# Optimization experiments

Measured on AMD Instinct MI355X. Metric: run time of the kernel, lower is better.

The kernel has to match this reference:

```python
import jax, jax.numpy as jnp
import numpy as np

NUM_GRAPHS = 512


def gcn_conv(x, W, b, src, dst, deg_inv_sqrt, n_nodes):
    # PyG GCNConv: out = D^{-1/2} (A+I) D^{-1/2} X W + b
    h = x @ W                                             # [N, F_out]
    norm = deg_inv_sqrt[src] * deg_inv_sqrt[dst]          # [E]
    msg = h[src] * norm[:, None]                          # gather + scale, [E, F_out]
    agg = jax.ops.segment_sum(msg, dst, num_segments=n_nodes)
    agg = agg + h * (deg_inv_sqrt ** 2)[:, None]          # self-loop term (norm = 1/deg)
    return agg + b


def setup_inputs() -> dict:
    key = jax.random.key(0)
    ks = jax.random.split(key, 8)
    N, E, F_in = 50000, 800000, 256
    hid2, out = 128, 64
    x = jax.random.normal(ks[0], (N, F_in), dtype=jnp.float32)
    edge_index = jax.random.randint(ks[1], (2, E), 0, N, dtype=jnp.int32)
    batch = jnp.sort(jax.random.randint(ks[2], (N,), 0, NUM_GRAPHS, dtype=jnp.int32))
    s = lambda k, sh: jax.random.normal(k, sh, dtype=jnp.float32) * (1.0 / np.sqrt(sh[0]))
    return {
        "x": x,
        "edge_index": edge_index,
        "batch": batch,
        "W1": s(ks[3], (F_in, hid2)), "b1": jnp.zeros((hid2,), jnp.float32),
        "W3": s(ks[4], (hid2, out)), "b3": jnp.zeros((out,), jnp.float32),
        "W4": s(ks[5], (hid2, out)), "b4": jnp.zeros((out,), jnp.float32),
        "Wfc": s(ks[6], (out, 4)), "bfc": jnp.zeros((4,), jnp.float32),
        "noise": jax.random.normal(ks[7], (N, out), dtype=jnp.float32),
    }


def reference(x, edge_index, batch, W1, b1, W3, b3, W4, b4, Wfc, bfc, noise):
    n_nodes = x.shape[0]
    src, dst = edge_index[0], edge_index[1]
    # degree of A + I (count of incoming edges per dst, plus self-loop)
    deg = jax.ops.segment_sum(jnp.ones_like(src, dtype=x.dtype), dst,
                              num_segments=n_nodes) + 1.0
    deg_inv_sqrt = jax.lax.rsqrt(deg)

    h = jax.nn.relu(gcn_conv(x, W1, b1, src, dst, deg_inv_sqrt, n_nodes))  # dropout p=0
    mean = gcn_conv(h, W3, b3, src, dst, deg_inv_sqrt, n_nodes)
    log_std = gcn_conv(h, W4, b4, src, dst, deg_inv_sqrt, n_nodes)
    z = mean + noise * jnp.exp(log_std)                   # reparametrize (training=True)

    # scatter_mean over graph ids
    sums = jax.ops.segment_sum(z, batch, num_segments=NUM_GRAPHS)
    counts = jax.ops.segment_sum(jnp.ones((n_nodes,), z.dtype), batch,
                                 num_segments=NUM_GRAPHS)
    pooled = sums / jnp.maximum(counts, 1.0)[:, None]     # [G, out]

    logits = pooled @ Wfc + bfc                           # [G, 4]
    return jax.nn.log_softmax(logits, axis=1)
```

## Files before the change

kernel.cpp:

```cpp
#include <hip/hip_runtime.h>
#include <hip/hip_bf16.h>
#include <cstdint>
#include <cmath>


typedef __attribute__((ext_vector_type(8))) short bf16x8;
typedef __attribute__((ext_vector_type(4))) float f32x4;

__device__ __forceinline__ unsigned short f2bf(float f) {
    union { float f; unsigned u; } v; v.f = f;
    unsigned u = v.u;
    return (unsigned short)((u + 0x7fffu + ((u >> 16) & 1u)) >> 16);
}
__device__ __forceinline__ float bf2f(unsigned b) {
    union { float f; unsigned u; } v; v.u = b << 16; return v.f;
}
__device__ __forceinline__ unsigned packbf(float lo, float hi) {
    return (unsigned)f2bf(lo) | ((unsigned)f2bf(hi) << 16);
}

__global__ __launch_bounds__(256) void deg_kernel(const int* __restrict__ dst,
                                                  int* __restrict__ deg, int E) {
    int e = blockIdx.x * 256 + threadIdx.x;
    if (e < E) atomicAdd(&deg[dst[e]], 1);
}

__global__ __launch_bounds__(256) void scan1_kernel(const int* __restrict__ deg,
                                                    int* __restrict__ bsum, int N) {
    int t = threadIdx.x;
    int base = blockIdx.x * 1024 + t * 4;
    int s = 0;
    if (base + 3 < N) {
        int4 v = *(const int4*)(deg + base);
        s = v.x + v.y + v.z + v.w;
    } else {
        for (int i = 0; i < 4; i++) if (base + i < N) s += deg[base + i];
    }
    __shared__ int red[256];
    red[t] = s;
    __syncthreads();
    for (int off = 128; off > 0; off >>= 1) {
        if (t < off) red[t] += red[t + off];
        __syncthreads();
    }
    if (t == 0) bsum[blockIdx.x] = red[0];
}

__global__ __launch_bounds__(256) void scan2_kernel(int* __restrict__ bsum, int nb) {
    __shared__ int s[256];
    int t = threadIdx.x;
    s[t] = (t < nb) ? bsum[t] : 0;
    __syncthreads();
    for (int off = 1; off < 256; off <<= 1) {
        int u = (t >= off) ? s[t - off] : 0;
        __syncthreads();
        s[t] += u;
        __syncthreads();
    }
    if (t < nb) bsum[t] = (t == 0) ? 0 : s[t - 1];
}

__global__ __launch_bounds__(256) void scan3_kernel(const int* __restrict__ deg,
                                                    const int* __restrict__ bsum,
                                                    int* __restrict__ offs,
                                                    int* __restrict__ cursor,
                                                    float* __restrict__ dis,
                                                    int N, int E) {
    int t = threadIdx.x;
    int bid = blockIdx.x;
    int base = bid * 1024 + t * 4;
    int d[4] = {0, 0, 0, 0};
    if (base + 3 < N) {
        int4 v = *(const int4*)(deg + base);
        d[0] = v.x; d[1] = v.y; d[2] = v.z; d[3] = v.w;
    } else {
        for (int i = 0; i < 4; i++) if (base + i < N) d[i] = deg[base + i];
    }
    int s = d[0] + d[1] + d[2] + d[3];
    __shared__ int red[256];
    red[t] = s;
    __syncthreads();
    for (int off = 1; off < 256; off <<= 1) {
        int u = (t >= off) ? red[t - off] : 0;
        __syncthreads();
        red[t] += u;
        __syncthreads();
    }
    int run = bsum[bid] + ((t == 0) ? 0 : red[t - 1]);
#pragma unroll
    for (int i = 0; i < 4; i++) {
        int idx = base + i;
        if (idx < N) {
            offs[idx] = run;
            cursor[idx] = run;
            dis[idx] = rsqrtf((float)d[i] + 1.0f);
            run += d[i];
        }
    }
    if (bid == 0 && t == 0) offs[N] = E;
}

__global__ __launch_bounds__(256) void fill_kernel(const int* __restrict__ src,
                                                   const int* __restrict__ dst,
                                                   int* __restrict__ cursor,
                                                   int* __restrict__ adj, int E) {
    int e = blockIdx.x * 256 + threadIdx.x;
    if (e >= E) return;
    int pos = atomicAdd(&cursor[dst[e]], 1);
    adj[pos] = src[e];
}

__global__ __launch_bounds__(256) void wt_kernel(const float* __restrict__ W,
                                                 unsigned short* __restrict__ wT) {
    int idx = blockIdx.x * 256 + threadIdx.x;
    if (idx < 32768) {
        int k = idx >> 7;
        int c = idx & 127;
        wT[c * 256 + k] = f2bf(W[idx]);
    }
}

__global__ __launch_bounds__(256) void gemm1_mfma(const float* __restrict__ x,
                                                  const unsigned short* __restrict__ wT,
                                                  const float* __restrict__ dis,
                                                  unsigned short* __restrict__ Abf,
                                                  float* __restrict__ B, int N) {
    __shared__ unsigned short xs[64 * 264];
    int tid = threadIdx.x;
    int rowBase = blockIdx.x * 64;
#pragma unroll
    for (int i = 0; i < 16; i++) {
        int u = tid + i * 256;
        int r = u >> 6;
        int c = u & 63;
        float4 v = make_float4(0.f, 0.f, 0.f, 0.f);
        int row = rowBase + r;
        if (row < N) v = *(const float4*)(x + (size_t)row * 256 + c * 4);
        ushort4 b;
        b.x = f2bf(v.x); b.y = f2bf(v.y); b.z = f2bf(v.z); b.w = f2bf(v.w);
        *(ushort4*)&xs[r * 264 + c * 4] = b;
    }
    __syncthreads();

    int wv = tid >> 6;
    int l = tid & 63;
    int lr = l & 15;
    int lk = l >> 4;
    int colBase = wv * 32;

    f32x4 acc[4][2];
#pragma unroll
    for (int rt = 0; rt < 4; rt++)
#pragma unroll
        for (int ct = 0; ct < 2; ct++) acc[rt][ct] = (f32x4){0.f, 0.f, 0.f, 0.f};

    for (int ks = 0; ks < 8; ks++) {
        int kbase = ks * 32 + lk * 8;
        bf16x8 a[4], b[2];
#pragma unroll
        for (int rt = 0; rt < 4; rt++)
            a[rt] = *(const bf16x8*)&xs[(rt * 16 + lr) * 264 + kbase];
#pragma unroll
        for (int ct = 0; ct < 2; ct++)
            b[ct] = *(const bf16x8*)(wT + (size_t)(colBase + ct * 16 + lr) * 256 + kbase);
#pragma unroll
        for (int rt = 0; rt < 4; rt++)
#pragma unroll
            for (int ct = 0; ct < 2; ct++)
                acc[rt][ct] = __builtin_amdgcn_mfma_f32_16x16x32_bf16(
                    a[rt], b[ct], acc[rt][ct], 0, 0, 0);
    }

#pragma unroll
    for (int rt = 0; rt < 4; rt++) {
#pragma unroll
        for (int j = 0; j < 4; j++) {
            int row = rowBase + rt * 16 + lk * 4 + j;
            if (row >= N) continue;
            float dv = dis[row];
            float d2 = dv * dv;
#pragma unroll
            for (int ct = 0; ct < 2; ct++) {
                int col = colBase + ct * 16 + lr;
                float v = acc[rt][ct][j];
                Abf[(size_t)row * 128 + col] = f2bf(v * dv);
                B[(size_t)row * 128 + col] = v * d2;
            }
        }
    }
}

template <int MODE>
__global__ __launch_bounds__(256) void gather_kernel(const int* __restrict__ offs,
                                                     const int* __restrict__ adj,
                                                     const float* __restrict__ dis,
                                                     const float* __restrict__ b1,
                                                     const unsigned short* __restrict__ Ain,
                                                     unsigned short* __restrict__ Aout,
                                                     float* __restrict__ B, int N) {
    int tid = threadIdx.x;
    int lane = tid & 15;
    int node = blockIdx.x * 16 + (tid >> 4);
    if (node >= N) return;
    int beg = offs[node];
    int end = offs[node + 1];
    float a[8];
#pragma unroll
    for (int j = 0; j < 8; j++) a[j] = 0.f;
    int e = beg;
    for (; e + 3 < end; e += 4) {
        int s0 = adj[e], s1 = adj[e + 1], s2 = adj[e + 2], s3 = adj[e + 3];
        uint4 r0 = ((const uint4*)(Ain + (size_t)s0 * 128))[lane];
        uint4 r1 = ((const uint4*)(Ain + (size_t)s1 * 128))[lane];
        uint4 r2 = ((const uint4*)(Ain + (size_t)s2 * 128))[lane];
        uint4 r3 = ((const uint4*)(Ain + (size_t)s3 * 128))[lane];
        a[0] += bf2f(r0.x & 0xffffu) + bf2f(r1.x & 0xffffu) + bf2f(r2.x & 0xffffu) + bf2f(r3.x & 0xffffu);
        a[1] += bf2f(r0.x >> 16)     + bf2f(r1.x >> 16)     + bf2f(r2.x >> 16)     + bf2f(r3.x >> 16);
        a[2] += bf2f(r0.y & 0xffffu) + bf2f(r1.y & 0xffffu) + bf2f(r2.y & 0xffffu) + bf2f(r3.y & 0xffffu);
        a[3] += bf2f(r0.y >> 16)     + bf2f(r1.y >> 16)     + bf2f(r2.y >> 16)     + bf2f(r3.y >> 16);
        a[4] += bf2f(r0.z & 0xffffu) + bf2f(r1.z & 0xffffu) + bf2f(r2.z & 0xffffu) + bf2f(r3.z & 0xffffu);
        a[5] += bf2f(r0.z >> 16)     + bf2f(r1.z >> 16)     + bf2f(r2.z >> 16)     + bf2f(r3.z >> 16);
        a[6] += bf2f(r0.w & 0xffffu) + bf2f(r1.w & 0xffffu) + bf2f(r2.w & 0xffffu) + bf2f(r3.w & 0xffffu);
        a[7] += bf2f(r0.w >> 16)     + bf2f(r1.w >> 16)     + bf2f(r2.w >> 16)     + bf2f(r3.w >> 16);
    }
    for (; e < end; e++) {
        int s = adj[e];
        uint4 r0 = ((const uint4*)(Ain + (size_t)s * 128))[lane];
        a[0] += bf2f(r0.x & 0xffffu);
        a[1] += bf2f(r0.x >> 16);
        a[2] += bf2f(r0.y & 0xffffu);
        a[3] += bf2f(r0.y >> 16);
        a[4] += bf2f(r0.z & 0xffffu);
        a[5] += bf2f(r0.z >> 16);
        a[6] += bf2f(r0.w & 0xffffu);
        a[7] += bf2f(r0.w >> 16);
    }
    float dd = dis[node];
    float* brow = B + (size_t)node * 128 + lane * 8;
    float4 cur0 = *(float4*)brow;
    float4 cur1 = *(float4*)(brow + 4);
    if (MODE == 0) {
        cur0.x += dd * a[0]; cur0.y += dd * a[1]; cur0.z += dd * a[2]; cur0.w += dd * a[3];
        cur1.x += dd * a[4]; cur1.y += dd * a[5]; cur1.z += dd * a[6]; cur1.w += dd * a[7];
        *(float4*)brow = cur0;
        *(float4*)(brow + 4) = cur1;
    } else {
        const float* b1p = b1 + lane * 8;
        float4 bb0 = *(const float4*)b1p;
        float4 bb1 = *(const float4*)(b1p + 4);
        float v0 = fmaxf(cur0.x + dd * a[0] + bb0.x, 0.f);
        float v1 = fmaxf(cur0.y + dd * a[1] + bb0.y, 0.f);
        float v2 = fmaxf(cur0.z + dd * a[2] + bb0.z, 0.f);
        float v3 = fmaxf(cur0.w + dd * a[3] + bb0.w, 0.f);
        float v4 = fmaxf(cur1.x + dd * a[4] + bb1.x, 0.f);
        float v5 = fmaxf(cur1.y + dd * a[5] + bb1.y, 0.f);
        float v6 = fmaxf(cur1.z + dd * a[6] + bb1.z, 0.f);
        float v7 = fmaxf(cur1.w + dd * a[7] + bb1.w, 0.f);
        uint4 w;
        w.x = packbf(v0 * dd, v1 * dd);
        w.y = packbf(v2 * dd, v3 * dd);
        w.z = packbf(v4 * dd, v5 * dd);
        w.w = packbf(v6 * dd, v7 * dd);
        *(uint4*)(Aout + (size_t)node * 128 + lane * 8) = w;
        float d2 = dd * dd;
        *(float4*)brow       = make_float4(v0 * d2, v1 * d2, v2 * d2, v3 * d2);
        *(float4*)(brow + 4) = make_float4(v4 * d2, v5 * d2, v6 * d2, v7 * d2);
    }
}

__device__ __forceinline__ int lbound_lds(const int* a, int n, int v) {
    int l = 0, r = n;
    while (l < r) { int m = (l + r) >> 1; if (a[m] < v) l = m + 1; else r = m; }
    return l;
}

__global__ __launch_bounds__(256) void pool2_kernel(const float* __restrict__ hagg,
                                                    const float* __restrict__ W4,
                                                    const float* __restrict__ b4,
                                                    const float* __restrict__ noise,
                                                    const int* __restrict__ batch,
                                                    float* __restrict__ pooledH,
                                                    float* __restrict__ pooledT,
                                                    int N) {
    __shared__ float xs[64][132];
    __shared__ float ws[128][64];
    __shared__ int sbatch[64];
    int tid = threadIdx.x;
    int rowBase = blockIdx.x * 64;
    int nrows = min(64, N - rowBase);

#pragma unroll
    for (int i = 0; i < 32; i++)
        ((float4*)ws)[tid + i * 256] = ((const float4*)W4)[tid + i * 256];
#pragma unroll
    for (int i = 0; i < 8; i++) {
        int u = tid + i * 256;
        int r = u >> 5;
        int c = u & 31;
        int row = rowBase + r;
        float4 v = make_float4(0.f, 0.f, 0.f, 0.f);
        if (row < N) v = *(const float4*)(hagg + (size_t)row * 128 + c * 4);
        *(float4*)&xs[r][c * 4] = v;
    }
    if (tid < 64) {
        int row = rowBase + tid;
        sbatch[tid] = (row < N) ? batch[row] : 0x7fffffff;
    }
    __syncthreads();

    int tx = tid & 15;
    int ty = tid >> 4;
    float acc[4][4];
#pragma unroll
    for (int i = 0; i < 4; i++)
#pragma unroll
        for (int j = 0; j < 4; j++) acc[i][j] = 0.f;
#pragma unroll 8
    for (int k = 0; k < 128; k++) {
        float xv[4];
#pragma unroll
        for (int i = 0; i < 4; i++) xv[i] = xs[ty * 4 + i][k];
        float4 wv = *(float4*)&ws[k][tx * 4];
        float w[4] = {wv.x, wv.y, wv.z, wv.w};
#pragma unroll
        for (int i = 0; i < 4; i++)
#pragma unroll
            for (int j = 0; j < 4; j++) acc[i][j] = fmaf(xv[i], w[j], acc[i][j]);
    }
    __syncthreads();

    int g0 = sbatch[0];
    int g1 = (nrows > 0) ? sbatch[nrows - 1] : g0;

    for (int g = g0; g <= g1; g++) {
        int lo = lbound_lds(sbatch, nrows, g);
        int hi = lbound_lds(sbatch, nrows, g + 1);
        if (hi > lo && tid < 128) {
            float s = 0.f;
            for (int r = lo; r < hi; r++) s += xs[r][tid];
            atomicAdd(&pooledH[g * 128 + tid], s);
        }
    }
    __syncthreads();

    float4 b4v = *(const float4*)(b4 + tx * 4);
    float bb[4] = {b4v.x, b4v.y, b4v.z, b4v.w};
#pragma unroll
    for (int i = 0; i < 4; i++) {
        int row = rowBase + ty * 4 + i;
        if (row < N) {
            float4 nz = *(const float4*)(noise + (size_t)row * 64 + tx * 4);
            float nv[4] = {nz.x, nz.y, nz.z, nz.w};
#pragma unroll
            for (int j = 0; j < 4; j++)
                xs[ty * 4 + i][tx * 4 + j] = nv[j] * expf(acc[i][j] + bb[j]);
        }
    }
    __syncthreads();

    for (int g = g0; g <= g1; g++) {
        int lo = lbound_lds(sbatch, nrows, g);
        int hi = lbound_lds(sbatch, nrows, g + 1);
        if (hi > lo && tid < 64) {
            float s = 0.f;
            for (int r = lo; r < hi; r++) s += xs[r][tid];
            atomicAdd(&pooledT[g * 64 + tid], s);
        }
    }
}

__global__ __launch_bounds__(64) void final_kernel(const float* __restrict__ pooledH,
                                                   const float* __restrict__ pooledT,
                                                   const int* __restrict__ batch,
                                                   const float* __restrict__ W3,
                                                   const float* __restrict__ b3,
                                                   const float* __restrict__ Wfc,
                                                   const float* __restrict__ bfc,
                                                   float* __restrict__ out, int N) {
    int g = blockIdx.x;
    int f = threadIdx.x;
    __shared__ int seg[2];
    if (f < 2) {
        int target = g + f;
        int l = 0, r = N;
        while (l < r) { int m = (l + r) >> 1; if (batch[m] < target) l = m + 1; else r = m; }
        seg[f] = l;
    }
    __syncthreads();
    float cnt = (float)(seg[1] - seg[0]);
    float denom = fmaxf(cnt, 1.0f);
    float p = pooledT[g * 64 + f] + cnt * b3[f];
    const float* ph = pooledH + g * 128;
#pragma unroll
    for (int k = 0; k < 128; k++) p = fmaf(ph[k], W3[k * 64 + f], p);
    p /= denom;
    __shared__ float pl[64];
    __shared__ float lg[4];
    pl[f] = p;
    __syncthreads();
    if (f < 4) {
        float l = bfc[f];
#pragma unroll
        for (int k = 0; k < 64; k++) l = fmaf(pl[k], Wfc[k * 4 + f], l);
        lg[f] = l;
    }
    __syncthreads();
    if (f == 0) {
        float m = fmaxf(fmaxf(lg[0], lg[1]), fmaxf(lg[2], lg[3]));
        float s = expf(lg[0] - m) + expf(lg[1] - m) + expf(lg[2] - m) + expf(lg[3] - m);
        float lse = logf(s);
#pragma unroll
        for (int j = 0; j < 4; j++) out[g * 4 + j] = lg[j] - m - lse;
    }
}

extern "C" void kernel_launch(void* const* d_in, const int* in_sizes, int n_in,
                              void* d_out, int out_size, void* d_ws, size_t ws_size,
                              hipStream_t stream) {
    const float* x     = (const float*)d_in[0];
    const int*   ei    = (const int*)d_in[1];
    const int*   batch = (const int*)d_in[2];
    const float* W1    = (const float*)d_in[3];
    const float* b1    = (const float*)d_in[4];
    const float* W3    = (const float*)d_in[5];
    const float* b3    = (const float*)d_in[6];
    const float* W4    = (const float*)d_in[7];
    const float* b4    = (const float*)d_in[8];
    const float* Wfc   = (const float*)d_in[9];
    const float* bfc   = (const float*)d_in[10];
    const float* noise = (const float*)d_in[11];
    float* out = (float*)d_out;

    int N = in_sizes[0] / 256;
    int E = in_sizes[1] / 2;
    const int* src = ei;
    const int* dst = ei + E;
    int nScanBlocks = (N + 1023) / 1024;

    float* B = (float*)d_ws;
    unsigned short* Abf = (unsigned short*)(B + (size_t)N * 128);
    unsigned short* wT  = Abf + (size_t)N * 128;
    float* dis     = (float*)(wT + 128 * 256);
    float* pooledH = dis + N;
    float* pooledT = pooledH + 512 * 128;
    int*   degi    = (int*)(pooledT + 512 * 64);
    int*   offs    = degi + N;
    int*   cursor  = offs + N + 1;
    int*   bsum    = cursor + N;
    int*   adj     = bsum + 256;

    hipMemsetAsync(degi, 0, (size_t)N * sizeof(int), stream);
    hipMemsetAsync(pooledH, 0, (size_t)(512 * 128 + 512 * 64) * sizeof(float), stream);

    deg_kernel<<<(E + 255) / 256, 256, 0, stream>>>(dst, degi, E);
    scan1_kernel<<<nScanBlocks, 256, 0, stream>>>(degi, bsum, N);
    scan2_kernel<<<1, 256, 0, stream>>>(bsum, nScanBlocks);
    scan3_kernel<<<nScanBlocks, 256, 0, stream>>>(degi, bsum, offs, cursor, dis, N, E);
    fill_kernel<<<(E + 255) / 256, 256, 0, stream>>>(src, dst, cursor, adj, E);
    wt_kernel<<<128, 256, 0, stream>>>(W1, wT);

    gemm1_mfma<<<(N + 63) / 64, 256, 0, stream>>>(x, wT, dis, Abf, B, N);

    gather_kernel<1><<<(N + 15) / 16, 256, 0, stream>>>(offs, adj, dis, b1, Abf, Abf, B, N);

    gather_kernel<0><<<(N + 15) / 16, 256, 0, stream>>>(offs, adj, dis, b1, Abf, Abf, B, N);

    pool2_kernel<<<(N + 63) / 64, 256, 0, stream>>>(B, W4, b4, noise, batch,
                                                    pooledH, pooledT, N);

    final_kernel<<<512, 64, 0, stream>>>(pooledH, pooledT, batch, W3, b3, Wfc, bfc, out, N);
}
```

Before: 343.8 us.

## Use bf16 MFMA for the log_std projection and split graph pooling

The second-layer aggregate gets an extra bf16 copy, and the 128x64 log_std projection now runs on MFMA instructions from a pre-transposed bf16 W4 instead of an FP32 LDS-tiled loop. Pooling of the hidden aggregate moves to a separate per-graph kernel that sums contiguous node ranges with no atomics. The CSR fill now uses nontemporal stores. This removes FP32 FMA work and LDS staging from the pool kernel, at the cost of an extra N x 128 bf16 write, an added launch, and reduced precision in the exp input.

```diff
diff --git a/kernel.cpp b/kernel.cpp
--- a/kernel.cpp
+++ b/kernel.cpp
@@ -107,7 +107,7 @@
     int e = blockIdx.x * 256 + threadIdx.x;
     if (e >= E) return;
     int pos = atomicAdd(&cursor[dst[e]], 1);
-    adj[pos] = src[e];
+    __builtin_nontemporal_store(src[e], &adj[pos]);
 }
 
 __global__ __launch_bounds__(256) void wt_kernel(const float* __restrict__ W,
@@ -117,6 +117,16 @@
         int k = idx >> 7;
         int c = idx & 127;
         wT[c * 256 + k] = f2bf(W[idx]);
+    }
+}
+
+__global__ __launch_bounds__(256) void wt4_kernel(const float* __restrict__ W4,
+                                                  unsigned short* __restrict__ w4T) {
+    int idx = blockIdx.x * 256 + threadIdx.x;
+    if (idx < 8192) {
+        int k = idx >> 6;
+        int c = idx & 63;
+        w4T[c * 128 + k] = f2bf(W4[idx]);
     }
 }
 
@@ -197,7 +207,8 @@
                                                      const float* __restrict__ b1,
                                                      const unsigned short* __restrict__ Ain,
                                                      unsigned short* __restrict__ Aout,
-                                                     float* __restrict__ B, int N) {
+                                                     float* __restrict__ B,
+                                                     unsigned short* __restrict__ Bbf, int N) {
     int tid = threadIdx.x;
     int lane = tid & 15;
     int node = blockIdx.x * 16 + (tid >> 4);
@@ -244,6 +255,12 @@
         cur1.x += dd * a[4]; cur1.y += dd * a[5]; cur1.z += dd * a[6]; cur1.w += dd * a[7];
         *(float4*)brow = cur0;
         *(float4*)(brow + 4) = cur1;
+        uint4 w;
+        w.x = packbf(cur0.x, cur0.y);
+        w.y = packbf(cur0.z, cur0.w);
+        w.z = packbf(cur1.x, cur1.y);
+        w.w = packbf(cur1.z, cur1.w);
+        *(uint4*)(Bbf + (size_t)node * 128 + lane * 8) = w;
     } else {
         const float* b1p = b1 + lane * 8;
         float4 bb0 = *(const float4*)b1p;
@@ -274,99 +291,86 @@
     return l;
 }
 
-__global__ __launch_bounds__(256) void pool2_kernel(const float* __restrict__ hagg,
-                                                    const float* __restrict__ W4,
-                                                    const float* __restrict__ b4,
-                                                    const float* __restrict__ noise,
-                                                    const int* __restrict__ batch,
-                                                    float* __restrict__ pooledH,
-                                                    float* __restrict__ pooledT,
-                                                    int N) {
-    __shared__ float xs[64][132];
-    __shared__ float ws[128][64];
+__global__ __launch_bounds__(256) void pool2_mfma(const unsigned short* __restrict__ Bbf,
+                                                  const unsigned short* __restrict__ w4T,
+                                                  const float* __restrict__ b4,
+                                                  const float* __restrict__ noise,
+                                                  const int* __restrict__ batch,
+                                                  float* __restrict__ pooledT, int N) {
+    __shared__ float Tld[64][68];
     __shared__ int sbatch[64];
     int tid = threadIdx.x;
     int rowBase = blockIdx.x * 64;
     int nrows = min(64, N - rowBase);
-
-#pragma unroll
-    for (int i = 0; i < 32; i++)
-        ((float4*)ws)[tid + i * 256] = ((const float4*)W4)[tid + i * 256];
-#pragma unroll
-    for (int i = 0; i < 8; i++) {
-        int u = tid + i * 256;
-        int r = u >> 5;
-        int c = u & 31;
-        int row = rowBase + r;
-        float4 v = make_float4(0.f, 0.f, 0.f, 0.f);
-        if (row < N) v = *(const float4*)(hagg + (size_t)row * 128 + c * 4);
-        *(float4*)&xs[r][c * 4] = v;
-    }
-    if (tid < 64) {
-        int row = rowBase + tid;
-        sbatch[tid] = (row < N) ? batch[row] : 0x7fffffff;
-    }
-    __syncthreads();
-
-    int tx = tid & 15;
-    int ty = tid >> 4;
-    float acc[4][4];
-#pragma unroll
-    for (int i = 0; i < 4; i++)
-#pragma unroll
-        for (int j = 0; j < 4; j++) acc[i][j] = 0.f;
-#pragma unroll 8
-    for (int k = 0; k < 128; k++) {
-        float xv[4];
-#pragma unroll
-        for (int i = 0; i < 4; i++) xv[i] = xs[ty * 4 + i][k];
-        float4 wv = *(float4*)&ws[k][tx * 4];
-        float w[4] = {wv.x, wv.y, wv.z, wv.w};
-#pragma unroll
-        for (int i = 0; i < 4; i++)
-#pragma unroll
-            for (int j = 0; j < 4; j++) acc[i][j] = fmaf(xv[i], w[j], acc[i][j]);
+    if (tid < 64) sbatch[tid] = (rowBase + tid < N) ? batch[rowBase + tid] : 0x7fffffff;
+
+    int wv = tid >> 6;
+    int l = tid & 63;
+    int lr = l & 15;
+    int lk = l >> 4;
+    int col = wv * 16 + lr;
+
+    f32x4 acc[4];
+#pragma unroll
+    for (int rt = 0; rt < 4; rt++) acc[rt] = (f32x4){0.f, 0.f, 0.f, 0.f};
+
+#pragma unroll
+    for (int ks = 0; ks < 4; ks++) {
+        int kbase = ks * 32 + lk * 8;
+        bf16x8 b = *(const bf16x8*)(w4T + (size_t)col * 128 + kbase);
+#pragma unroll
+        for (int rt = 0; rt < 4; rt++) {
+            int row = rowBase + rt * 16 + lr;
+            bf16x8 a = {0, 0, 0, 0, 0, 0, 0, 0};
+            if (row < N) a = *(const bf16x8*)(Bbf + (size_t)row * 128 + kbase);
+            acc[rt] = __builtin_amdgcn_mfma_f32_16x16x32_bf16(a, b, acc[rt], 0, 0, 0);
+        }
+    }
+    __syncthreads();
+
+    float bv = b4[col];
+#pragma unroll
+    for (int rt = 0; rt < 4; rt++) {
+#pragma unroll
+        for (int j = 0; j < 4; j++) {
+            int r = rt * 16 + lk * 4 + j;
+            int row = rowBase + r;
+            if (row < N)
+                Tld[r][col] = noise[(size_t)row * 64 + col] * expf(acc[rt][j] + bv);
+        }
     }
     __syncthreads();
 
     int g0 = sbatch[0];
     int g1 = (nrows > 0) ? sbatch[nrows - 1] : g0;
-
-    for (int g = g0; g <= g1; g++) {
-        int lo = lbound_lds(sbatch, nrows, g);
-        int hi = lbound_lds(sbatch, nrows, g + 1);
-        if (hi > lo && tid < 128) {
-            float s = 0.f;
-            for (int r = lo; r < hi; r++) s += xs[r][tid];
-            atomicAdd(&pooledH[g * 128 + tid], s);
-        }
-    }
-    __syncthreads();
-
-    float4 b4v = *(const float4*)(b4 + tx * 4);
-    float bb[4] = {b4v.x, b4v.y, b4v.z, b4v.w};
-#pragma unroll
-    for (int i = 0; i < 4; i++) {
-        int row = rowBase + ty * 4 + i;
-        if (row < N) {
-            float4 nz = *(const float4*)(noise + (size_t)row * 64 + tx * 4);
-            float nv[4] = {nz.x, nz.y, nz.z, nz.w};
-#pragma unroll
-            for (int j = 0; j < 4; j++)
-                xs[ty * 4 + i][tx * 4 + j] = nv[j] * expf(acc[i][j] + bb[j]);
-        }
-    }
-    __syncthreads();
-
     for (int g = g0; g <= g1; g++) {
         int lo = lbound_lds(sbatch, nrows, g);
         int hi = lbound_lds(sbatch, nrows, g + 1);
         if (hi > lo && tid < 64) {
             float s = 0.f;
-            for (int r = lo; r < hi; r++) s += xs[r][tid];
+            for (int r = lo; r < hi; r++) s += Tld[r][tid];
             atomicAdd(&pooledT[g * 64 + tid], s);
         }
     }
+}
+
+__global__ __launch_bounds__(128) void poolH_kernel(const float* __restrict__ B,
+                                                    const int* __restrict__ batch,
+                                                    float* __restrict__ pooledH, int N) {
+    int g = blockIdx.x;
+    int f = threadIdx.x;
+    __shared__ int seg[2];
+    if (f < 2) {
+        int target = g + f;
+        int l = 0, r = N;
+        while (l < r) { int m = (l + r) >> 1; if (batch[m] < target) l = m + 1; else r = m; }
+        seg[f] = l;
+    }
+    __syncthreads();
+    float s = 0.f;
+    for (int node = seg[0]; node < seg[1]; node++)
+        s += B[(size_t)node * 128 + f];
+    pooledH[g * 128 + f] = s;
 }
 
 __global__ __launch_bounds__(64) void final_kernel(const float* __restrict__ pooledH,
@@ -439,8 +443,10 @@
 
     float* B = (float*)d_ws;
     unsigned short* Abf = (unsigned short*)(B + (size_t)N * 128);
-    unsigned short* wT  = Abf + (size_t)N * 128;
-    float* dis     = (float*)(wT + 128 * 256);
+    unsigned short* Bbf = Abf + (size_t)N * 128;
+    unsigned short* wT  = Bbf + (size_t)N * 128;
+    unsigned short* w4T = wT + 128 * 256;
+    float* dis     = (float*)(w4T + 64 * 128);
     float* pooledH = dis + N;
     float* pooledT = pooledH + 512 * 128;
     int*   degi    = (int*)(pooledT + 512 * 64);
@@ -450,7 +456,7 @@
     int*   adj     = bsum + 256;
 
     hipMemsetAsync(degi, 0, (size_t)N * sizeof(int), stream);
-    hipMemsetAsync(pooledH, 0, (size_t)(512 * 128 + 512 * 64) * sizeof(float), stream);
+    hipMemsetAsync(pooledT, 0, (size_t)(512 * 64) * sizeof(float), stream);
 
     deg_kernel<<<(E + 255) / 256, 256, 0, stream>>>(dst, degi, E);
     scan1_kernel<<<nScanBlocks, 256, 0, stream>>>(degi, bsum, N);
@@ -458,15 +464,16 @@
     scan3_kernel<<<nScanBlocks, 256, 0, stream>>>(degi, bsum, offs, cursor, dis, N, E);
     fill_kernel<<<(E + 255) / 256, 256, 0, stream>>>(src, dst, cursor, adj, E);
     wt_kernel<<<128, 256, 0, stream>>>(W1, wT);
+    wt4_kernel<<<32, 256, 0, stream>>>(W4, w4T);
 
     gemm1_mfma<<<(N + 63) / 64, 256, 0, stream>>>(x, wT, dis, Abf, B, N);
 
-    gather_kernel<1><<<(N + 15) / 16, 256, 0, stream>>>(offs, adj, dis, b1, Abf, Abf, B, N);
-
-    gather_kernel<0><<<(N + 15) / 16, 256, 0, stream>>>(offs, adj, dis, b1, Abf, Abf, B, N);
-
-    pool2_kernel<<<(N + 63) / 64, 256, 0, stream>>>(B, W4, b4, noise, batch,
-                                                    pooledH, pooledT, N);
+    gather_kernel<1><<<(N + 15) / 16, 256, 0, stream>>>(offs, adj, dis, b1, Abf, Abf, B, Bbf, N);
+
+    gather_kernel<0><<<(N + 15) / 16, 256, 0, stream>>>(offs, adj, dis, b1, Abf, Abf, B, Bbf, N);
+
+    pool2_mfma<<<(N + 63) / 64, 256, 0, stream>>>(Bbf, w4T, b4, noise, batch, pooledT, N);
+    poolH_kernel<<<512, 128, 0, stream>>>(B, batch, pooledH, N);
 
     final_kernel<<<512, 64, 0, stream>>>(pooledH, pooledT, batch, W3, b3, Wfc, bfc, out, N);
 }
```

Result: slower. 374.6 us (+9.0%).
